# Kernel optimization log

Measured on AMD Instinct MI355X. Metric: run time of the kernel, lower is better.

Reference implementation:

```python
import jax, jax.numpy as jnp
import numpy as np

INPUT, HIDDEN, OUTPUT = 512, 1024, 256
BATCH, SEQ = 128, 512


def setup_inputs() -> dict:
    key = jax.random.key(0)
    ks = jax.random.split(key, 8)
    s_in = 1.0 / np.sqrt(INPUT)
    s_h = 1.0 / np.sqrt(HIDDEN)
    return {
        "x": jax.random.normal(ks[0], (BATCH, SEQ, INPUT), dtype=jnp.float32),
        "W_in": jax.random.uniform(ks[1], (INPUT, HIDDEN), jnp.float32, -s_in, s_in),
        "b_in": jax.random.uniform(ks[2], (HIDDEN,), jnp.float32, -s_in, s_in),
        "W_h": jax.random.uniform(ks[3], (HIDDEN, HIDDEN), jnp.float32, -s_h, s_h),
        "b_h": jax.random.uniform(ks[4], (HIDDEN,), jnp.float32, -s_h, s_h),
        "tau": jnp.ones((HIDDEN,), jnp.float32),
        "W_out": jax.random.uniform(ks[5], (HIDDEN, OUTPUT), jnp.float32, -s_h, s_h),
        "b_out": jax.random.uniform(ks[6], (OUTPUT,), jnp.float32, -s_h, s_h),
    }


def reference(x, W_in, b_in, W_h, b_h, tau, W_out, b_out):
    # Precompute input projections for all timesteps in one big GEMM: [B,S,H]
    xin = jnp.einsum('bsi,ih->bsh', x, W_in) + b_in

    def step(h, xin_t):
        dx = jnp.tanh(xin_t + h @ W_h + b_h)
        h_new = h + (dx - h) / tau
        return h_new, None

    h0 = jnp.zeros((x.shape[0], W_h.shape[0]), x.dtype)
    h_final, _ = jax.lax.scan(step, h0, jnp.swapaxes(xin, 0, 1))
    return h_final @ W_out + b_out
```

## Files before the change

kernel.cpp:

```cpp
#include <hip/hip_runtime.h>
#include <hip/hip_fp16.h>

typedef _Float16 half8 __attribute__((ext_vector_type(8)));
typedef float floatx4 __attribute__((ext_vector_type(4)));
typedef unsigned int uintx4 __attribute__((ext_vector_type(4)));

#define INPUT  512
#define HIDDEN 1024
#define OUTPUT 256
#define BATCH  128
#define SEQ    512

__global__ __launch_bounds__(256) void transpose_f32_to_f16(
    const float* __restrict__ in, _Float16* __restrict__ out, int K, int N) {
  __shared__ float tile[32][33];
  int bi = blockIdx.x;
  int bj = blockIdx.y;
  int cc = threadIdx.x & 31;
  int rr = threadIdx.x >> 5;
#pragma unroll
  for (int s = 0; s < 4; ++s) {
    int r = rr + 8 * s;
    tile[r][cc] = in[(size_t)(bi * 32 + r) * N + bj * 32 + cc];
  }
  __syncthreads();
#pragma unroll
  for (int s = 0; s < 4; ++s) {
    int nl = rr + 8 * s;
    out[(size_t)(bj * 32 + nl) * K + bi * 32 + cc] = (_Float16)tile[cc][nl];
  }
}

__global__ __launch_bounds__(256) void pack_win(
    const float* __restrict__ W, _Float16* __restrict__ P) {
  int idx = blockIdx.x * 256 + threadIdx.x;
  int k = idx >> 10, n = idx & 1023;
  P[((size_t)(k >> 5) << 15) + (n << 5) + (k & 31)] = (_Float16)W[idx];
}

__global__ __launch_bounds__(256) void xin_gemm(
    const float* __restrict__ x, const _Float16* __restrict__ WinP,
    _Float16* __restrict__ xin) {
  int bid = blockIdx.x;
  int bm = (bid & 7) * 128 + ((bid >> 3) & 127);
  int bn = bid >> 10;
  int tid = threadIdx.x;
  int l = tid & 63;
  int w = tid >> 6;
  int l15 = l & 15;
  int lk = (l >> 4) << 3;

  int rowbase = bm * 64 + w * 16;
  int colbase = bn * 128;

  floatx4 acc[8];
#pragma unroll
  for (int nt = 0; nt < 8; ++nt) acc[nt] = (floatx4){0.f, 0.f, 0.f, 0.f};

  const float* xrow = x + (size_t)(rowbase + l15) * INPUT;

  for (int k0 = 0; k0 < INPUT; k0 += 32) {
    int ak = k0 + lk;
    float4 xa = *reinterpret_cast<const float4*>(xrow + ak);
    float4 xb = *reinterpret_cast<const float4*>(xrow + ak + 4);
    half8 a;
    a[0] = (_Float16)xa.x; a[1] = (_Float16)xa.y;
    a[2] = (_Float16)xa.z; a[3] = (_Float16)xa.w;
    a[4] = (_Float16)xb.x; a[5] = (_Float16)xb.y;
    a[6] = (_Float16)xb.z; a[7] = (_Float16)xb.w;
    const _Float16* pq = WinP + ((size_t)(k0 >> 5) << 15) + l15 * 32 + lk;
#pragma unroll
    for (int nt = 0; nt < 8; ++nt) {
      half8 b = *reinterpret_cast<const half8*>(pq + (colbase + nt * 16) * 32);
      acc[nt] = __builtin_amdgcn_mfma_f32_16x16x32_f16(a, b, acc[nt], 0, 0, 0);
    }
  }

  int orow = rowbase + ((l >> 4) << 2);
#pragma unroll
  for (int nt = 0; nt < 8; ++nt)
#pragma unroll
    for (int i = 0; i < 4; ++i) {
      int r = orow + i;
      int b = r >> 9;
      int s = r & 511;
      xin[((size_t)s * BATCH + b) * HIDDEN + colbase + nt * 16 + l15] =
          (_Float16)acc[nt][i];
    }
}

__global__ __launch_bounds__(512) void liquid_scan(
    const _Float16* __restrict__ xin,
    const _Float16* __restrict__ WhT,
    const float* __restrict__ b_in, const float* __restrict__ b_h,
    const float* __restrict__ tau,
    unsigned int* hbuf,
    float* __restrict__ hfinal) {
  int blk = blockIdx.x;
  int m = blk & 7;
  int j = blk >> 3;
  int tid = threadIdx.x;
  int l = tid & 63;
  int w = tid >> 6;
  int g = w & 1;
  int kg = w >> 1;
  int l15 = l & 15;
  int lk = (l >> 4) << 3;

  __shared__ _Float16 Ald[16][1032];
  __shared__ float part[2][2][4][64][4];

  half8 wf0[8], wf1[8];
  {
    const _Float16* wb0 =
        WhT + (size_t)(j * 64 + g * 32 + l15) * HIDDEN + kg * 256 + lk;
    const _Float16* wb1 = wb0 + 16 * HIDDEN;
#pragma unroll
    for (int kt = 0; kt < 8; ++kt) {
      wf0[kt] = *reinterpret_cast<const half8*>(wb0 + kt * 32);
      wf1[kt] = *reinterpret_cast<const half8*>(wb1 + kt * 32);
    }
  }

  const int wp = tid >> 6;
  const int lp = tid & 63;
  const int gc = j * 64 + lp;
  const float bias_c = b_in[gc] + b_h[gc];
  const float invtau_c = 1.0f / tau[gc];
  float hown[2] = {0.f, 0.f};
  const int r0 = 2 * wp;
  const int gb0 = m * 16 + r0;

  const int ntg = lp >> 5;
  const int nt2 = (lp >> 4) & 1;
  const int lsrc0 = (((r0 + 0) >> 2) << 4) | (lp & 15);
  const int lsrc1 = (((r0 + 1) >> 2) << 4) | (lp & 15);
  const int i_0 = (r0 + 0) & 3;
  const int i_1 = (r0 + 1) & 3;

  const int srow = tid >> 8;
  const int scol4 = (tid & 255) * 4;
  unsigned int* gbase = hbuf + m * 16384 + tid * 4;

  _Float16 xc[2], x1[2], xn[2];
#pragma unroll
  for (int b = 0; b < 2; ++b) {
    xc[b] = xin[((size_t)0 * BATCH + gb0 + b) * HIDDEN + gc];
    x1[b] = xin[((size_t)1 * BATCH + gb0 + b) * HIDDEN + gc];
  }

  for (int t = 0; t < SEQ; ++t) {
    if (t > 0) {
      unsigned int* bp = gbase + (size_t)(t & 1) * 131072;
      const unsigned want = (unsigned)t;
      uintx4 q0, q1, q2, q3, q4, q5, q6, q7;
      for (;;) {
        asm volatile(
            "global_load_dwordx4 %0, %8, off sc1\n\t"
            "global_load_dwordx4 %1, %9, off sc1\n\t"
            "global_load_dwordx4 %2, %10, off sc1\n\t"
            "global_load_dwordx4 %3, %11, off sc1\n\t"
            "global_load_dwordx4 %4, %12, off sc1\n\t"
            "global_load_dwordx4 %5, %13, off sc1\n\t"
            "global_load_dwordx4 %6, %14, off sc1\n\t"
            "global_load_dwordx4 %7, %15, off sc1\n\t"
            "s_waitcnt vmcnt(0)"
            : "=&v"(q0), "=&v"(q1), "=&v"(q2), "=&v"(q3),
              "=&v"(q4), "=&v"(q5), "=&v"(q6), "=&v"(q7)
            : "v"(bp), "v"(bp + 2048), "v"(bp + 4096), "v"(bp + 6144),
              "v"(bp + 8192), "v"(bp + 10240), "v"(bp + 12288),
              "v"(bp + 14336)
            : "memory");
        unsigned bad = 0;
#define CH(Q) bad |= ((Q[0] ^ want) | (Q[1] ^ want) | (Q[2] ^ want) | \
                      (Q[3] ^ want)) & 0xFFFFu;
        CH(q0) CH(q1) CH(q2) CH(q3) CH(q4) CH(q5) CH(q6) CH(q7)
#undef CH
        if (!__any((int)(bad != 0u))) break;
      }
#define STRIP(Q, I)                                                          \
      {                                                                      \
        unsigned lo = __builtin_amdgcn_perm(Q[1], Q[0], 0x07060302u);        \
        unsigned hi = __builtin_amdgcn_perm(Q[3], Q[2], 0x07060302u);        \
        unsigned int* d =                                                    \
            reinterpret_cast<unsigned int*>(&Ald[2 * I + srow][scol4]);      \
        d[0] = lo; d[1] = hi;                                                \
      }
      STRIP(q0, 0) STRIP(q1, 1) STRIP(q2, 2) STRIP(q3, 3)
      STRIP(q4, 4) STRIP(q5, 5) STRIP(q6, 6) STRIP(q7, 7)
#undef STRIP
    }

    {
      const int ts = (t + 2 < SEQ) ? t + 2 : SEQ - 1;
      xn[0] = xin[((size_t)ts * BATCH + gb0) * HIDDEN + gc];
      xn[1] = xin[((size_t)ts * BATCH + gb0 + 1) * HIDDEN + gc];
    }
    __syncthreads();

    floatx4 acc0 = (floatx4){0.f, 0.f, 0.f, 0.f};
    floatx4 acc1 = (floatx4){0.f, 0.f, 0.f, 0.f};
    if (t > 0) {
      const int kb = kg * 256 + lk;
#pragma unroll
      for (int kt = 0; kt < 8; ++kt) {
        half8 a = *reinterpret_cast<const half8*>(&Ald[l15][kb + kt * 32]);
        acc0 = __builtin_amdgcn_mfma_f32_16x16x32_f16(a, wf0[kt], acc0, 0, 0, 0);
        acc1 = __builtin_amdgcn_mfma_f32_16x16x32_f16(a, wf1[kt], acc1, 0, 0, 0);
      }
    }
    {
      const int slot = (kg + (l >> 3)) & 3;
#pragma unroll
      for (int i = 0; i < 4; ++i) {
        part[g][0][i][l][slot] = acc0[i];
        part[g][1][i][l][slot] = acc1[i];
      }
    }
    __syncthreads();

    unsigned int* outb = hbuf + (size_t)((t + 1) & 1) * 131072 + m * 16384;
#pragma unroll
    for (int b = 0; b < 2; ++b) {
      const floatx4 p = *reinterpret_cast<const floatx4*>(
          &part[ntg][nt2][b ? i_1 : i_0][b ? lsrc1 : lsrc0][0]);
      const float s = (p[0] + p[1]) + (p[2] + p[3]);
      float pre = s + (float)xc[b] + bias_c;
      pre = fminf(fmaxf(pre, -15.f), 15.f);
      const float e = __expf(2.f * pre);
      const float dx = (e - 1.f) / (e + 1.f);
      const float hn = hown[b] + (dx - hown[b]) * invtau_c;
      hown[b] = hn;
      if (t < SEQ - 1) {
        const unsigned short hb =
            __builtin_bit_cast(unsigned short, (_Float16)hn);
        const unsigned word = ((unsigned)hb << 16) | (unsigned)(t + 1);
        __hip_atomic_store(outb + (r0 + b) * 1024 + gc, word,
                           __ATOMIC_RELAXED, __HIP_MEMORY_SCOPE_AGENT);
      } else {
        hfinal[(size_t)(gb0 + b) * HIDDEN + gc] = hn;
      }
    }
    xc[0] = x1[0]; xc[1] = x1[1];
    x1[0] = xn[0]; x1[1] = xn[1];
  }
}

__global__ __launch_bounds__(256) void out_gemm(
    const float* __restrict__ hfinal, const float* __restrict__ Wout,
    const float* __restrict__ bout, float* __restrict__ out) {
  int b0 = blockIdx.x * 2;
  int o = threadIdx.x;
  float a0 = 0.f, a1 = 0.f;
  for (int k = 0; k < HIDDEN; ++k) {
    float wv = Wout[(size_t)k * OUTPUT + o];
    a0 += hfinal[(size_t)b0 * HIDDEN + k] * wv;
    a1 += hfinal[(size_t)(b0 + 1) * HIDDEN + k] * wv;
  }
  out[(size_t)b0 * OUTPUT + o] = a0 + bout[o];
  out[(size_t)(b0 + 1) * OUTPUT + o] = a1 + bout[o];
}

extern "C" void kernel_launch(void* const* d_in, const int* in_sizes, int n_in,
                              void* d_out, int out_size, void* d_ws,
                              size_t ws_size, hipStream_t stream) {
  const float* x     = (const float*)d_in[0];
  const float* W_in  = (const float*)d_in[1];
  const float* b_in  = (const float*)d_in[2];
  const float* W_h   = (const float*)d_in[3];
  const float* b_h   = (const float*)d_in[4];
  const float* tau   = (const float*)d_in[5];
  const float* W_out = (const float*)d_in[6];
  const float* b_out = (const float*)d_in[7];
  float* out = (float*)d_out;

  char* ws = (char*)d_ws;
  _Float16* xin = (_Float16*)ws;  ws += (size_t)BATCH * SEQ * HIDDEN * 2;
  _Float16* WinP = (_Float16*)ws; ws += (size_t)INPUT * HIDDEN * 2;
  _Float16* WhT = (_Float16*)ws;  ws += (size_t)HIDDEN * HIDDEN * 2;
  unsigned int* hbuf = (unsigned int*)ws;
  ws += (size_t)2 * BATCH * HIDDEN * 4;
  float* hfin = (float*)ws;       ws += (size_t)BATCH * HIDDEN * 4;

  hipMemsetAsync(hbuf, 0, (size_t)2 * BATCH * HIDDEN * 4, stream);

  transpose_f32_to_f16<<<dim3(HIDDEN / 32, HIDDEN / 32), 256, 0, stream>>>(
      W_h, WhT, HIDDEN, HIDDEN);
  pack_win<<<(INPUT * HIDDEN) / 256, 256, 0, stream>>>(W_in, WinP);

  xin_gemm<<<(BATCH * SEQ / 64) * (HIDDEN / 128), 256, 0, stream>>>(x, WinP,
                                                                    xin);

  liquid_scan<<<128, 512, 0, stream>>>(xin, WhT, b_in, b_h, tau, hbuf, hfin);

  out_gemm<<<BATCH / 2, OUTPUT, 0, stream>>>(hfin, W_out, b_out, out);
}
```

Before: 1.408 ms.

## Load h fragments directly from global into registers, drop LDS staging barrier

Each wave now polls and loads exactly the h slice its MFMA A-fragments need straight from the global exchange buffer and packs it into half8 registers. This removes the shared-memory staging array and one __syncthreads per timestep. The partial-sum buffer is double-buffered by step parity so the remaining barrier is enough. The cost is that each wave polls twice as many dwords, and the 8 waves redundantly load overlapping h data, which adds global/L2 traffic and register pressure.

```diff
diff --git a/kernel.cpp b/kernel.cpp
--- a/kernel.cpp
+++ b/kernel.cpp
@@ -107,8 +107,7 @@
   int l15 = l & 15;
   int lk = (l >> 4) << 3;
 
-  __shared__ _Float16 Ald[16][1032];
-  __shared__ float part[2][2][4][64][4];
+  __shared__ float part[2][2][2][4][64][4];
 
   half8 wf0[8], wf1[8];
   {
@@ -130,7 +129,6 @@
   float hown[2] = {0.f, 0.f};
   const int r0 = 2 * wp;
   const int gb0 = m * 16 + r0;
-
   const int ntg = lp >> 5;
   const int nt2 = (lp >> 4) & 1;
   const int lsrc0 = (((r0 + 0) >> 2) << 4) | (lp & 15);
@@ -138,9 +136,7 @@
   const int i_0 = (r0 + 0) & 3;
   const int i_1 = (r0 + 1) & 3;
 
-  const int srow = tid >> 8;
-  const int scol4 = (tid & 255) * 4;
-  unsigned int* gbase = hbuf + m * 16384 + tid * 4;
+  unsigned int* gpoll = hbuf + m * 16384 + l15 * 1024 + kg * 256 + lk;
 
   _Float16 xc[2], x1[2], xn[2];
 #pragma unroll
@@ -150,45 +146,58 @@
   }
 
   for (int t = 0; t < SEQ; ++t) {
+    const int par = t & 1;
+    half8 hf0, hf1, hf2, hf3, hf4, hf5, hf6, hf7;
     if (t > 0) {
-      unsigned int* bp = gbase + (size_t)(t & 1) * 131072;
+      unsigned int* bp = gpoll + (size_t)(t & 1) * 131072;
       const unsigned want = (unsigned)t;
-      uintx4 q0, q1, q2, q3, q4, q5, q6, q7;
+      uintx4 q0, q1, q2, q3, q4, q5, q6, q7, q8, q9, qa, qb, qc, qd, qe, qf;
       for (;;) {
         asm volatile(
-            "global_load_dwordx4 %0, %8, off sc1\n\t"
-            "global_load_dwordx4 %1, %9, off sc1\n\t"
-            "global_load_dwordx4 %2, %10, off sc1\n\t"
-            "global_load_dwordx4 %3, %11, off sc1\n\t"
-            "global_load_dwordx4 %4, %12, off sc1\n\t"
-            "global_load_dwordx4 %5, %13, off sc1\n\t"
-            "global_load_dwordx4 %6, %14, off sc1\n\t"
-            "global_load_dwordx4 %7, %15, off sc1\n\t"
+            "global_load_dwordx4 %0, %16, off sc1\n\t"
+            "global_load_dwordx4 %1, %16, off offset:16 sc1\n\t"
+            "global_load_dwordx4 %2, %16, off offset:128 sc1\n\t"
+            "global_load_dwordx4 %3, %16, off offset:144 sc1\n\t"
+            "global_load_dwordx4 %4, %16, off offset:256 sc1\n\t"
+            "global_load_dwordx4 %5, %16, off offset:272 sc1\n\t"
+            "global_load_dwordx4 %6, %16, off offset:384 sc1\n\t"
+            "global_load_dwordx4 %7, %16, off offset:400 sc1\n\t"
+            "global_load_dwordx4 %8, %16, off offset:512 sc1\n\t"
+            "global_load_dwordx4 %9, %16, off offset:528 sc1\n\t"
+            "global_load_dwordx4 %10, %16, off offset:640 sc1\n\t"
+            "global_load_dwordx4 %11, %16, off offset:656 sc1\n\t"
+            "global_load_dwordx4 %12, %16, off offset:768 sc1\n\t"
+            "global_load_dwordx4 %13, %16, off offset:784 sc1\n\t"
+            "global_load_dwordx4 %14, %16, off offset:896 sc1\n\t"
+            "global_load_dwordx4 %15, %16, off offset:912 sc1\n\t"
             "s_waitcnt vmcnt(0)"
-            : "=&v"(q0), "=&v"(q1), "=&v"(q2), "=&v"(q3),
-              "=&v"(q4), "=&v"(q5), "=&v"(q6), "=&v"(q7)
-            : "v"(bp), "v"(bp + 2048), "v"(bp + 4096), "v"(bp + 6144),
-              "v"(bp + 8192), "v"(bp + 10240), "v"(bp + 12288),
-              "v"(bp + 14336)
+            : "=&v"(q0), "=&v"(q1), "=&v"(q2), "=&v"(q3), "=&v"(q4),
+              "=&v"(q5), "=&v"(q6), "=&v"(q7), "=&v"(q8), "=&v"(q9),
+              "=&v"(qa), "=&v"(qb), "=&v"(qc), "=&v"(qd), "=&v"(qe),
+              "=&v"(qf)
+            : "v"(bp)
             : "memory");
         unsigned bad = 0;
 #define CH(Q) bad |= ((Q[0] ^ want) | (Q[1] ^ want) | (Q[2] ^ want) | \
                       (Q[3] ^ want)) & 0xFFFFu;
         CH(q0) CH(q1) CH(q2) CH(q3) CH(q4) CH(q5) CH(q6) CH(q7)
+        CH(q8) CH(q9) CH(qa) CH(qb) CH(qc) CH(qd) CH(qe) CH(qf)
 #undef CH
         if (!__any((int)(bad != 0u))) break;
       }
-#define STRIP(Q, I)                                                          \
+#define MKFRAG(D, QA, QB)                                                    \
       {                                                                      \
-        unsigned lo = __builtin_amdgcn_perm(Q[1], Q[0], 0x07060302u);        \
-        unsigned hi = __builtin_amdgcn_perm(Q[3], Q[2], 0x07060302u);        \
-        unsigned int* d =                                                    \
-            reinterpret_cast<unsigned int*>(&Ald[2 * I + srow][scol4]);      \
-        d[0] = lo; d[1] = hi;                                                \
+        uintx4 u;                                                            \
+        u[0] = __builtin_amdgcn_perm(QA[1], QA[0], 0x07060302u);             \
+        u[1] = __builtin_amdgcn_perm(QA[3], QA[2], 0x07060302u);             \
+        u[2] = __builtin_amdgcn_perm(QB[1], QB[0], 0x07060302u);             \
+        u[3] = __builtin_amdgcn_perm(QB[3], QB[2], 0x07060302u);             \
+        D = __builtin_bit_cast(half8, u);                                    \
       }
-      STRIP(q0, 0) STRIP(q1, 1) STRIP(q2, 2) STRIP(q3, 3)
-      STRIP(q4, 4) STRIP(q5, 5) STRIP(q6, 6) STRIP(q7, 7)
-#undef STRIP
+      MKFRAG(hf0, q0, q1) MKFRAG(hf1, q2, q3) MKFRAG(hf2, q4, q5)
+      MKFRAG(hf3, q6, q7) MKFRAG(hf4, q8, q9) MKFRAG(hf5, qa, qb)
+      MKFRAG(hf6, qc, qd) MKFRAG(hf7, qe, qf)
+#undef MKFRAG
     }
 
     {
@@ -196,25 +205,33 @@
       xn[0] = xin[((size_t)ts * BATCH + gb0) * HIDDEN + gc];
       xn[1] = xin[((size_t)ts * BATCH + gb0 + 1) * HIDDEN + gc];
     }
-    __syncthreads();
 
     floatx4 acc0 = (floatx4){0.f, 0.f, 0.f, 0.f};
     floatx4 acc1 = (floatx4){0.f, 0.f, 0.f, 0.f};
     if (t > 0) {
-      const int kb = kg * 256 + lk;
-#pragma unroll
-      for (int kt = 0; kt < 8; ++kt) {
-        half8 a = *reinterpret_cast<const half8*>(&Ald[l15][kb + kt * 32]);
-        acc0 = __builtin_amdgcn_mfma_f32_16x16x32_f16(a, wf0[kt], acc0, 0, 0, 0);
-        acc1 = __builtin_amdgcn_mfma_f32_16x16x32_f16(a, wf1[kt], acc1, 0, 0, 0);
-      }
+      acc0 = __builtin_amdgcn_mfma_f32_16x16x32_f16(hf0, wf0[0], acc0, 0, 0, 0);
+      acc1 = __builtin_amdgcn_mfma_f32_16x16x32_f16(hf0, wf1[0], acc1, 0, 0, 0);
+      acc0 = __builtin_amdgcn_mfma_f32_16x16x32_f16(hf1, wf0[1], acc0, 0, 0, 0);
+      acc1 = __builtin_amdgcn_mfma_f32_16x16x32_f16(hf1, wf1[1], acc1, 0, 0, 0);
+      acc0 = __builtin_amdgcn_mfma_f32_16x16x32_f16(hf2, wf0[2], acc0, 0, 0, 0);
+      acc1 = __builtin_amdgcn_mfma_f32_16x16x32_f16(hf2, wf1[2], acc1, 0, 0, 0);
+      acc0 = __builtin_amdgcn_mfma_f32_16x16x32_f16(hf3, wf0[3], acc0, 0, 0, 0);
+      acc1 = __builtin_amdgcn_mfma_f32_16x16x32_f16(hf3, wf1[3], acc1, 0, 0, 0);
+      acc0 = __builtin_amdgcn_mfma_f32_16x16x32_f16(hf4, wf0[4], acc0, 0, 0, 0);
+      acc1 = __builtin_amdgcn_mfma_f32_16x16x32_f16(hf4, wf1[4], acc1, 0, 0, 0);
+      acc0 = __builtin_amdgcn_mfma_f32_16x16x32_f16(hf5, wf0[5], acc0, 0, 0, 0);
+      acc1 = __builtin_amdgcn_mfma_f32_16x16x32_f16(hf5, wf1[5], acc1, 0, 0, 0);
+      acc0 = __builtin_amdgcn_mfma_f32_16x16x32_f16(hf6, wf0[6], acc0, 0, 0, 0);
+      acc1 = __builtin_amdgcn_mfma_f32_16x16x32_f16(hf6, wf1[6], acc1, 0, 0, 0);
+      acc0 = __builtin_amdgcn_mfma_f32_16x16x32_f16(hf7, wf0[7], acc0, 0, 0, 0);
+      acc1 = __builtin_amdgcn_mfma_f32_16x16x32_f16(hf7, wf1[7], acc1, 0, 0, 0);
     }
     {
       const int slot = (kg + (l >> 3)) & 3;
 #pragma unroll
       for (int i = 0; i < 4; ++i) {
-        part[g][0][i][l][slot] = acc0[i];
-        part[g][1][i][l][slot] = acc1[i];
+        part[par][g][0][i][l][slot] = acc0[i];
+        part[par][g][1][i][l][slot] = acc1[i];
       }
     }
     __syncthreads();
@@ -223,7 +240,7 @@
 #pragma unroll
     for (int b = 0; b < 2; ++b) {
       const floatx4 p = *reinterpret_cast<const floatx4*>(
-          &part[ntg][nt2][b ? i_1 : i_0][b ? lsrc1 : lsrc0][0]);
+          &part[par][ntg][nt2][b ? i_1 : i_0][b ? lsrc1 : lsrc0][0]);
       const float s = (p[0] + p[1]) + (p[2] + p[3]);
       float pre = s + (float)xc[b] + bias_c;
       pre = fminf(fmaxf(pre, -15.f), 15.f);
```

Measured after the change: 2.869 ms. 104% more time.

## Fuse input projection GEMM into the recurrent scan kernel

Applied to the files above, without the earlier changes.

Removes the separate xin GEMM and its half-precision intermediate buffer. Each scan block now keeps a slice of W_in in registers, loads the fp32 x rows for the next timestep, stages them in LDS as fp16, and adds the input projection into the same MFMA accumulators as the recurrent product. This drops the large xin write and read traffic and one kernel launch. In exchange, the input-projection MFMAs and the x loads now sit on the serial critical path of every timestep, and register pressure per thread goes up.

```diff
diff --git a/kernel.cpp b/kernel.cpp
--- a/kernel.cpp
+++ b/kernel.cpp
@@ -31,67 +31,10 @@
   }
 }
 
-__global__ __launch_bounds__(256) void pack_win(
-    const float* __restrict__ W, _Float16* __restrict__ P) {
-  int idx = blockIdx.x * 256 + threadIdx.x;
-  int k = idx >> 10, n = idx & 1023;
-  P[((size_t)(k >> 5) << 15) + (n << 5) + (k & 31)] = (_Float16)W[idx];
-}
-
-__global__ __launch_bounds__(256) void xin_gemm(
-    const float* __restrict__ x, const _Float16* __restrict__ WinP,
-    _Float16* __restrict__ xin) {
-  int bid = blockIdx.x;
-  int bm = (bid & 7) * 128 + ((bid >> 3) & 127);
-  int bn = bid >> 10;
-  int tid = threadIdx.x;
-  int l = tid & 63;
-  int w = tid >> 6;
-  int l15 = l & 15;
-  int lk = (l >> 4) << 3;
-
-  int rowbase = bm * 64 + w * 16;
-  int colbase = bn * 128;
-
-  floatx4 acc[8];
-#pragma unroll
-  for (int nt = 0; nt < 8; ++nt) acc[nt] = (floatx4){0.f, 0.f, 0.f, 0.f};
-
-  const float* xrow = x + (size_t)(rowbase + l15) * INPUT;
-
-  for (int k0 = 0; k0 < INPUT; k0 += 32) {
-    int ak = k0 + lk;
-    float4 xa = *reinterpret_cast<const float4*>(xrow + ak);
-    float4 xb = *reinterpret_cast<const float4*>(xrow + ak + 4);
-    half8 a;
-    a[0] = (_Float16)xa.x; a[1] = (_Float16)xa.y;
-    a[2] = (_Float16)xa.z; a[3] = (_Float16)xa.w;
-    a[4] = (_Float16)xb.x; a[5] = (_Float16)xb.y;
-    a[6] = (_Float16)xb.z; a[7] = (_Float16)xb.w;
-    const _Float16* pq = WinP + ((size_t)(k0 >> 5) << 15) + l15 * 32 + lk;
-#pragma unroll
-    for (int nt = 0; nt < 8; ++nt) {
-      half8 b = *reinterpret_cast<const half8*>(pq + (colbase + nt * 16) * 32);
-      acc[nt] = __builtin_amdgcn_mfma_f32_16x16x32_f16(a, b, acc[nt], 0, 0, 0);
-    }
-  }
-
-  int orow = rowbase + ((l >> 4) << 2);
-#pragma unroll
-  for (int nt = 0; nt < 8; ++nt)
-#pragma unroll
-    for (int i = 0; i < 4; ++i) {
-      int r = orow + i;
-      int b = r >> 9;
-      int s = r & 511;
-      xin[((size_t)s * BATCH + b) * HIDDEN + colbase + nt * 16 + l15] =
-          (_Float16)acc[nt][i];
-    }
-}
-
 __global__ __launch_bounds__(512) void liquid_scan(
-    const _Float16* __restrict__ xin,
+    const float* __restrict__ x,
     const _Float16* __restrict__ WhT,
+    const _Float16* __restrict__ WinT,
     const float* __restrict__ b_in, const float* __restrict__ b_h,
     const float* __restrict__ tau,
     unsigned int* hbuf,
@@ -108,9 +51,10 @@
   int lk = (l >> 4) << 3;
 
   __shared__ _Float16 Ald[16][1032];
+  __shared__ _Float16 Xld[16][520];
   __shared__ float part[2][2][4][64][4];
 
-  half8 wf0[8], wf1[8];
+  half8 wf0[8], wf1[8], wi0[4], wi1[4];
   {
     const _Float16* wb0 =
         WhT + (size_t)(j * 64 + g * 32 + l15) * HIDDEN + kg * 256 + lk;
@@ -119,6 +63,14 @@
     for (int kt = 0; kt < 8; ++kt) {
       wf0[kt] = *reinterpret_cast<const half8*>(wb0 + kt * 32);
       wf1[kt] = *reinterpret_cast<const half8*>(wb1 + kt * 32);
+    }
+    const _Float16* vb0 =
+        WinT + (size_t)(j * 64 + g * 32 + l15) * INPUT + kg * 128 + lk;
+    const _Float16* vb1 = vb0 + 16 * INPUT;
+#pragma unroll
+    for (int kt = 0; kt < 4; ++kt) {
+      wi0[kt] = *reinterpret_cast<const half8*>(vb0 + kt * 32);
+      wi1[kt] = *reinterpret_cast<const half8*>(vb1 + kt * 32);
     }
   }
 
@@ -130,7 +82,6 @@
   float hown[2] = {0.f, 0.f};
   const int r0 = 2 * wp;
   const int gb0 = m * 16 + r0;
-
   const int ntg = lp >> 5;
   const int nt2 = (lp >> 4) & 1;
   const int lsrc0 = (((r0 + 0) >> 2) << 4) | (lp & 15);
@@ -142,12 +93,14 @@
   const int scol4 = (tid & 255) * 4;
   unsigned int* gbase = hbuf + m * 16384 + tid * 4;
 
-  _Float16 xc[2], x1[2], xn[2];
-#pragma unroll
-  for (int b = 0; b < 2; ++b) {
-    xc[b] = xin[((size_t)0 * BATCH + gb0 + b) * HIDDEN + gc];
-    x1[b] = xin[((size_t)1 * BATCH + gb0 + b) * HIDDEN + gc];
-  }
+  const int rx = tid >> 5;
+  const int cx = (tid & 31) * 16;
+  const float* xrow =
+      x + ((size_t)(m * 16 + rx) * SEQ) * INPUT + cx;
+  float4 xv4[4];
+#pragma unroll
+  for (int p = 0; p < 4; ++p)
+    xv4[p] = *reinterpret_cast<const float4*>(xrow + 0 * INPUT + p * 4);
 
   for (int t = 0; t < SEQ; ++t) {
     if (t > 0) {
@@ -192,9 +145,21 @@
     }
 
     {
-      const int ts = (t + 2 < SEQ) ? t + 2 : SEQ - 1;
-      xn[0] = xin[((size_t)ts * BATCH + gb0) * HIDDEN + gc];
-      xn[1] = xin[((size_t)ts * BATCH + gb0 + 1) * HIDDEN + gc];
+      half8 h0, h1;
+#pragma unroll
+      for (int e = 0; e < 4; ++e) {
+        h0[e]     = (_Float16)xv4[0][e];
+        h0[e + 4] = (_Float16)xv4[1][e];
+        h1[e]     = (_Float16)xv4[2][e];
+        h1[e + 4] = (_Float16)xv4[3][e];
+      }
+      *reinterpret_cast<half8*>(&Xld[rx][cx]) = h0;
+      *reinterpret_cast<half8*>(&Xld[rx][cx + 8]) = h1;
+      const int ts = (t + 1 < SEQ) ? t + 1 : SEQ - 1;
+      const float* xp = xrow + (size_t)ts * INPUT;
+#pragma unroll
+      for (int p = 0; p < 4; ++p)
+        xv4[p] = *reinterpret_cast<const float4*>(xp + p * 4);
     }
     __syncthreads();
 
@@ -210,6 +175,15 @@
       }
     }
     {
+      const int xb = kg * 128 + lk;
+#pragma unroll
+      for (int kt = 0; kt < 4; ++kt) {
+        half8 a = *reinterpret_cast<const half8*>(&Xld[l15][xb + kt * 32]);
+        acc0 = __builtin_amdgcn_mfma_f32_16x16x32_f16(a, wi0[kt], acc0, 0, 0, 0);
+        acc1 = __builtin_amdgcn_mfma_f32_16x16x32_f16(a, wi1[kt], acc1, 0, 0, 0);
+      }
+    }
+    {
       const int slot = (kg + (l >> 3)) & 3;
 #pragma unroll
       for (int i = 0; i < 4; ++i) {
@@ -225,7 +199,7 @@
       const floatx4 p = *reinterpret_cast<const floatx4*>(
           &part[ntg][nt2][b ? i_1 : i_0][b ? lsrc1 : lsrc0][0]);
       const float s = (p[0] + p[1]) + (p[2] + p[3]);
-      float pre = s + (float)xc[b] + bias_c;
+      float pre = s + bias_c;
       pre = fminf(fmaxf(pre, -15.f), 15.f);
       const float e = __expf(2.f * pre);
       const float dx = (e - 1.f) / (e + 1.f);
@@ -241,8 +215,6 @@
         hfinal[(size_t)(gb0 + b) * HIDDEN + gc] = hn;
       }
     }
-    xc[0] = x1[0]; xc[1] = x1[1];
-    x1[0] = xn[0]; x1[1] = xn[1];
   }
 }
 
@@ -275,8 +247,7 @@
   float* out = (float*)d_out;
 
   char* ws = (char*)d_ws;
-  _Float16* xin = (_Float16*)ws;  ws += (size_t)BATCH * SEQ * HIDDEN * 2;
-  _Float16* WinP = (_Float16*)ws; ws += (size_t)INPUT * HIDDEN * 2;
+  _Float16* WinT = (_Float16*)ws; ws += (size_t)HIDDEN * INPUT * 2;
   _Float16* WhT = (_Float16*)ws;  ws += (size_t)HIDDEN * HIDDEN * 2;
   unsigned int* hbuf = (unsigned int*)ws;
   ws += (size_t)2 * BATCH * HIDDEN * 4;
@@ -286,12 +257,11 @@
 
   transpose_f32_to_f16<<<dim3(HIDDEN / 32, HIDDEN / 32), 256, 0, stream>>>(
       W_h, WhT, HIDDEN, HIDDEN);
-  pack_win<<<(INPUT * HIDDEN) / 256, 256, 0, stream>>>(W_in, WinP);
-
-  xin_gemm<<<(BATCH * SEQ / 64) * (HIDDEN / 128), 256, 0, stream>>>(x, WinP,
-                                                                    xin);
-
-  liquid_scan<<<128, 512, 0, stream>>>(xin, WhT, b_in, b_h, tau, hbuf, hfin);
+  transpose_f32_to_f16<<<dim3(INPUT / 32, HIDDEN / 32), 256, 0, stream>>>(
+      W_in, WinT, INPUT, HIDDEN);
+
+  liquid_scan<<<128, 512, 0, stream>>>(x, WhT, WinT, b_in, b_h, tau, hbuf,
+                                       hfin);
 
   out_gemm<<<BATCH / 2, OUTPUT, 0, stream>>>(hfin, W_out, b_out, out);
 }
```

Result: slower. 1.603 ms (+13.9%).
